# Kernel tuning notes

Measured on AMD Instinct MI355X. Metric: run time of the kernel, lower is better.

Reference implementation:

```python
import jax, jax.numpy as jnp
import numpy as np

N_NODES = 100000
N_EDGES = 1600000
N_FEAT = 128
HIDDEN = 128
N_CLASSES = 64


def setup_inputs() -> dict:
    key = jax.random.key(0)
    ks = jax.random.split(key, 6)
    x = jax.random.normal(ks[0], (N_NODES, N_FEAT), dtype=jnp.float32)
    edge_index = jax.random.randint(ks[1], (2, N_EDGES), 0, N_NODES, dtype=jnp.int64)
    # Glorot-ish scaled weights
    W1_l = jax.random.normal(ks[2], (N_FEAT, HIDDEN), dtype=jnp.float32) / np.sqrt(N_FEAT)
    W1_r = jax.random.normal(ks[3], (N_FEAT, HIDDEN), dtype=jnp.float32) / np.sqrt(N_FEAT)
    W2_l = jax.random.normal(ks[4], (HIDDEN, N_CLASSES), dtype=jnp.float32) / np.sqrt(HIDDEN)
    W2_r = jax.random.normal(ks[5], (HIDDEN, N_CLASSES), dtype=jnp.float32) / np.sqrt(HIDDEN)
    b1 = jnp.zeros((HIDDEN,), dtype=jnp.float32)
    b2 = jnp.zeros((N_CLASSES,), dtype=jnp.float32)
    return {"x": x, "edge_index": edge_index, "W1_l": W1_l, "b1": b1,
            "W1_r": W1_r, "W2_l": W2_l, "b2": b2, "W2_r": W2_r}


def _sage_conv(h, src, dst, n_nodes, inv_deg, W_l, W_r, b):
    # mean aggregation of source-node features into destination nodes
    agg = jax.ops.segment_sum(h[src], dst, num_segments=n_nodes)  # [N, d]
    agg = agg * inv_deg[:, None]
    return agg @ W_l + h @ W_r + b


def reference(x, edge_index, W1_l, b1, W1_r, W2_l, b2, W2_r):
    src, dst = edge_index[0], edge_index[1]
    n = x.shape[0]
    deg = jax.ops.segment_sum(jnp.ones_like(dst, dtype=x.dtype), dst, num_segments=n)
    inv_deg = 1.0 / jnp.maximum(deg, 1.0)
    h = jax.nn.relu(_sage_conv(x, src, dst, n, inv_deg, W1_l, W1_r, b1))
    # dropout is identity in eval mode
    out = _sage_conv(h, src, dst, n, inv_deg, W2_l, W2_r, b2)
    return out
```

## Files before the change

kernel.cpp:

```cpp
#include <hip/hip_runtime.h>

#define N_NODES   100000
#define N_EDGES   1600000
#define BSHIFT    9
#define NB        196

typedef __attribute__((ext_vector_type(8))) short short8;
typedef __attribute__((ext_vector_type(4))) float f32x4;
typedef __attribute__((ext_vector_type(2))) float f32x2;

__device__ __forceinline__ unsigned short f2bf(float f) {
    unsigned u = __float_as_uint(f);
    u += 0x7FFF + ((u >> 16) & 1);
    return (unsigned short)(u >> 16);
}

__device__ __forceinline__ int load_src(const int* e, int is64, int i) {
    return is64 ? e[2 * i] : e[i];
}
__device__ __forceinline__ int load_dst(const int* e, int is64, int i) {
    return is64 ? e[2 * (N_EDGES + i)] : e[N_EDGES + i];
}

__device__ __forceinline__ int block_detect_is64(const int* e, int* s_nz) {
    if (threadIdx.x == 0) *s_nz = 0;
    __syncthreads();
    int v = 0;
    for (int i = threadIdx.x; i < 1024; i += 256) v |= e[2 * i + 1];
    if (v) atomicOr(s_nz, 1);
    __syncthreads();
    return (*s_nz == 0) ? 1 : 0;
}

__global__ __launch_bounds__(256) void phaseA_kernel(
        const int* __restrict__ e, const float* __restrict__ x,
        const float* __restrict__ W1_l, const float* __restrict__ W1_r,
        const float* __restrict__ W2_l, const float* __restrict__ W2_r,
        int* __restrict__ bcnt, short* __restrict__ xb,
        unsigned int* __restrict__ xq,
        short* __restrict__ W1t, short* __restrict__ W2lt, short* __restrict__ W2rt) {
    const int blk = blockIdx.x;
    if (blk < 391) {
        __shared__ int s_nz;
        __shared__ int s_cnt[NB];
        for (int t = threadIdx.x; t < NB; t += 256) s_cnt[t] = 0;
        int is64 = block_detect_is64(e, &s_nz);
        __syncthreads();
        int i0 = blk * 4096;
        int n = min(4096, N_EDGES - i0);
        for (int t = 0; t < 16; t++) {
            int k = t * 256 + threadIdx.x;
            if (k < n) {
                int d = load_dst(e, is64, i0 + k);
                atomicAdd(&s_cnt[d >> BSHIFT], 1);
            }
        }
        __syncthreads();
        for (int t = threadIdx.x; t < NB; t += 256)
            if (s_cnt[t]) atomicAdd(&bcnt[t], s_cnt[t]);
    } else if (blk < 12891) {
        int t = (blk - 391) * 256 + threadIdx.x;
        int i = t * 4;
        float4 v = *(const float4*)&x[i];
        short4 o;
        o.x = (short)f2bf(v.x); o.y = (short)f2bf(v.y);
        o.z = (short)f2bf(v.z); o.w = (short)f2bf(v.w);
        *(short4*)&xb[i] = o;
        int w = __builtin_amdgcn_cvt_pk_fp8_f32(v.x, v.y, 0, false);
        w = __builtin_amdgcn_cvt_pk_fp8_f32(v.z, v.w, w, true);
        xq[t] = (unsigned int)w;
    } else {
        int i = (blk - 12891) * 256 + threadIdx.x;
        if (i < 32768) {
            int n = i >> 8, k = i & 255;
            float v = (k < 128) ? W1_l[k * 128 + n] : W1_r[(k - 128) * 128 + n];
            W1t[i] = (short)f2bf(v);
        } else if (i < 40960) {
            int j = i - 32768, n = j >> 7, k = j & 127;
            W2lt[j] = (short)f2bf(W2_l[k * 64 + n]);
        } else {
            int j = i - 40960, n = j >> 7, k = j & 127;
            W2rt[j] = (short)f2bf(W2_r[k * 64 + n]);
        }
    }
}

__global__ __launch_bounds__(256) void binscat_kernel(
        const int* __restrict__ e, const int* __restrict__ bcnt,
        int* __restrict__ boff, int* __restrict__ pairs) {
    __shared__ int2 s_pairs[4096];
    __shared__ int s_cnt[256], s_off[256], s_base[256], s_cur[256];
    __shared__ int s_nz;
    const int tid = threadIdx.x;
    s_cnt[tid] = 0;
    int is64 = block_detect_is64(e, &s_nz);
    __syncthreads();
    int i0 = blockIdx.x * 4096;
    int n = min(4096, N_EDGES - i0);
    int ls[16], ld[16];
    #pragma unroll
    for (int t = 0; t < 16; t++) {
        int k = t * 256 + tid;
        if (k < n) {
            ls[t] = load_src(e, is64, i0 + k);
            ld[t] = load_dst(e, is64, i0 + k);
            atomicAdd(&s_cnt[ld[t] >> BSHIFT], 1);
        }
    }
    __syncthreads();
    int lv = s_cnt[tid];
    s_off[tid] = lv;
    __syncthreads();
    for (int off = 1; off < 256; off <<= 1) {
        int t = (tid >= off) ? s_off[tid - off] : 0;
        __syncthreads();
        s_off[tid] += t;
        __syncthreads();
    }
    int excl = s_off[tid] - lv;
    int gv = (tid < NB) ? bcnt[tid] : 0;
    s_base[tid] = gv;
    __syncthreads();
    for (int off = 1; off < 256; off <<= 1) {
        int t = (tid >= off) ? s_base[tid - off] : 0;
        __syncthreads();
        s_base[tid] += t;
        __syncthreads();
    }
    int bst = s_base[tid] - gv;
    int gb = 0;
    if (tid < NB && lv > 0) gb = atomicAdd(&boff[tid], lv);
    s_off[tid] = excl;
    s_base[tid] = bst + gb;
    s_cur[tid] = excl;
    __syncthreads();
    #pragma unroll
    for (int t = 0; t < 16; t++) {
        int k = t * 256 + tid;
        if (k < n) {
            int pos = atomicAdd(&s_cur[ld[t] >> BSHIFT], 1);
            s_pairs[pos] = (int2){ls[t], ld[t]};
        }
    }
    __syncthreads();
    for (int j = tid; j < n; j += 256) {
        int2 pr = s_pairs[j];
        int b = pr.y >> BSHIFT;
        pairs[s_base[b] + (j - s_off[b])] = pr.x | ((pr.y & 511) << 17);
    }
}

__global__ __launch_bounds__(256) void fused_fill_kernel(
        const int* __restrict__ bcnt, const int* __restrict__ pairs,
        int* __restrict__ deg_i, int* __restrict__ cursor,
        float* __restrict__ inv_deg, int* __restrict__ col) {
    __shared__ int ldeg[512];
    __shared__ int ssum[256];
    __shared__ int sp0;
    const int tid = threadIdx.x;
    const int b = blockIdx.x;
    const int nbase = b << BSHIFT;
    int gv = (tid < NB) ? bcnt[tid] : 0;
    ssum[tid] = gv;
    __syncthreads();
    for (int off = 1; off < 256; off <<= 1) {
        int t = (tid >= off) ? ssum[tid - off] : 0;
        __syncthreads();
        ssum[tid] += t;
        __syncthreads();
    }
    if (tid == b) sp0 = ssum[tid] - gv;
    ldeg[tid] = 0; ldeg[tid + 256] = 0;
    __syncthreads();
    const int p0 = sp0, cnt = bcnt[b];
    for (int j = tid; j < cnt; j += 256)
        atomicAdd(&ldeg[pairs[p0 + j] >> 17], 1);
    __syncthreads();
    int d0 = ldeg[tid * 2], d1 = ldeg[tid * 2 + 1];
    int tsum = d0 + d1;
    ssum[tid] = tsum;
    __syncthreads();
    for (int off = 1; off < 256; off <<= 1) {
        int t = (tid >= off) ? ssum[tid - off] : 0;
        __syncthreads();
        ssum[tid] += t;
        __syncthreads();
    }
    int excl = ssum[tid] - tsum;
    int s0 = p0 + excl;
    int s1 = s0 + d0;
    ldeg[tid * 2] = s0;
    ldeg[tid * 2 + 1] = s1;
    int idx0 = nbase + tid * 2;
    if (idx0 < N_NODES) {
        deg_i[idx0] = d0;
        cursor[idx0] = s0;
        inv_deg[idx0] = 1.0f / fmaxf((float)d0, 1.0f);
    }
    if (idx0 + 1 < N_NODES) {
        deg_i[idx0 + 1] = d1;
        cursor[idx0 + 1] = s1;
        inv_deg[idx0 + 1] = 1.0f / fmaxf((float)d1, 1.0f);
    }
    __syncthreads();
    for (int j = tid; j < cnt; j += 256) {
        int pk = pairs[p0 + j];
        int pos = atomicAdd(&ldeg[pk >> 17], 1);
        col[pos] = pk & 0x1FFFF;
    }
}

__device__ __forceinline__ void acc_fp8x8(float* acc, uint2 w) {
    f32x2 f;
    f = __builtin_amdgcn_cvt_pk_f32_fp8((int)w.x, false); acc[0] += f[0]; acc[1] += f[1];
    f = __builtin_amdgcn_cvt_pk_f32_fp8((int)w.x, true);  acc[2] += f[0]; acc[3] += f[1];
    f = __builtin_amdgcn_cvt_pk_f32_fp8((int)w.y, false); acc[4] += f[0]; acc[5] += f[1];
    f = __builtin_amdgcn_cvt_pk_f32_fp8((int)w.y, true);  acc[6] += f[0]; acc[7] += f[1];
}

__global__ __launch_bounds__(256) void agg128_kernel(
        const int* __restrict__ cursor, const int* __restrict__ deg_i,
        const int* __restrict__ col, const unsigned int* __restrict__ xq,
        const float* __restrict__ inv_deg, short* __restrict__ agg) {
    int node = blockIdx.x * 16 + (threadIdx.x >> 4);
    int lane = threadIdx.x & 15;
    int cnt = deg_i[node];
    int start = cursor[node];
    float acc[8] = {0.f};
    int k = 0;
    for (; k + 4 <= cnt; k += 4) {
        int s0 = col[start + k + 0];
        int s1 = col[start + k + 1];
        int s2 = col[start + k + 2];
        int s3 = col[start + k + 3];
        uint2 w0 = *(const uint2*)(xq + (size_t)s0 * 32 + lane * 2);
        uint2 w1 = *(const uint2*)(xq + (size_t)s1 * 32 + lane * 2);
        uint2 w2 = *(const uint2*)(xq + (size_t)s2 * 32 + lane * 2);
        uint2 w3 = *(const uint2*)(xq + (size_t)s3 * 32 + lane * 2);
        acc_fp8x8(acc, w0); acc_fp8x8(acc, w1);
        acc_fp8x8(acc, w2); acc_fp8x8(acc, w3);
    }
    for (; k < cnt; k++) {
        int s0 = col[start + k];
        uint2 w = *(const uint2*)(xq + (size_t)s0 * 32 + lane * 2);
        acc_fp8x8(acc, w);
    }
    float sc = inv_deg[node];
    short8 o;
    #pragma unroll
    for (int j = 0; j < 8; j++) o[j] = (short)f2bf(acc[j] * sc);
    *(short8*)(agg + (size_t)node * 128 + lane * 8) = o;
}

__global__ __launch_bounds__(256) void agg64_kernel(
        const int* __restrict__ cursor, const int* __restrict__ deg_i,
        const int* __restrict__ col, const unsigned int* __restrict__ pq,
        const float* __restrict__ inv_deg, float* __restrict__ out) {
    int node = blockIdx.x * 32 + (threadIdx.x >> 3);
    int lane = threadIdx.x & 7;
    int cnt = deg_i[node];
    int start = cursor[node];
    float acc[8] = {0.f};
    int k = 0;
    for (; k + 4 <= cnt; k += 4) {
        int s0 = col[start + k + 0];
        int s1 = col[start + k + 1];
        int s2 = col[start + k + 2];
        int s3 = col[start + k + 3];
        uint2 w0 = *(const uint2*)(pq + (size_t)s0 * 16 + lane * 2);
        uint2 w1 = *(const uint2*)(pq + (size_t)s1 * 16 + lane * 2);
        uint2 w2 = *(const uint2*)(pq + (size_t)s2 * 16 + lane * 2);
        uint2 w3 = *(const uint2*)(pq + (size_t)s3 * 16 + lane * 2);
        acc_fp8x8(acc, w0); acc_fp8x8(acc, w1);
        acc_fp8x8(acc, w2); acc_fp8x8(acc, w3);
    }
    for (; k < cnt; k++) {
        int s0 = col[start + k];
        uint2 w = *(const uint2*)(pq + (size_t)s0 * 16 + lane * 2);
        acc_fp8x8(acc, w);
    }
    float sc = inv_deg[node];
    float* dst = out + (size_t)node * 64 + lane * 8;
    float4 o0 = *(float4*)dst;
    float4 o1 = *(float4*)(dst + 4);
    o0.x += acc[0] * sc; o0.y += acc[1] * sc; o0.z += acc[2] * sc; o0.w += acc[3] * sc;
    o1.x += acc[4] * sc; o1.y += acc[5] * sc; o1.z += acc[6] * sc; o1.w += acc[7] * sc;
    *(float4*)dst = o0;
    *(float4*)(dst + 4) = o1;
}

__global__ __launch_bounds__(256, 2) void gemm1_mfma(
        const short* __restrict__ agg1, const short* __restrict__ xb,
        const short* __restrict__ W1t, const float* __restrict__ b1,
        short* __restrict__ h) {
    const int wave = threadIdx.x >> 6, lane = threadIdx.x & 63;
    const int m = lane & 15, q = lane >> 4;
    const int wid = blockIdx.x * 4 + wave;
    const int half = wid & 1;
    short8 breg[4][8];
    #pragma unroll
    for (int t = 0; t < 4; t++)
        #pragma unroll
        for (int c = 0; c < 8; c++)
            breg[t][c] = *(const short8*)(W1t + (size_t)(half * 64 + t * 16 + m) * 256 + c * 32 + q * 8);
    float bias[4];
    #pragma unroll
    for (int t = 0; t < 4; t++) bias[t] = b1[half * 64 + t * 16 + m];

    for (int tile = wid >> 1; tile < 6250; tile += 1024) {
        const short* arow = agg1 + (size_t)(tile * 16 + m) * 128;
        const short* xrow = xb + (size_t)(tile * 16 + m) * 128;
        short8 a[8];
        #pragma unroll
        for (int c = 0; c < 4; c++) a[c] = *(const short8*)(arow + c * 32 + q * 8);
        #pragma unroll
        for (int c = 0; c < 4; c++) a[c + 4] = *(const short8*)(xrow + c * 32 + q * 8);
        f32x4 acc[4];
        #pragma unroll
        for (int t = 0; t < 4; t++) acc[t] = (f32x4){0.f, 0.f, 0.f, 0.f};
        #pragma unroll
        for (int c = 0; c < 8; c++)
            #pragma unroll
            for (int t = 0; t < 4; t++)
                acc[t] = __builtin_amdgcn_mfma_f32_16x16x32_bf16(a[c], breg[t][c], acc[t], 0, 0, 0);
        #pragma unroll
        for (int t = 0; t < 4; t++) {
            int colc = half * 64 + t * 16 + m;
            #pragma unroll
            for (int r = 0; r < 4; r++) {
                int rr = tile * 16 + q * 4 + r;
                h[(size_t)rr * 128 + colc] = (short)f2bf(fmaxf(acc[t][r] + bias[t], 0.f));
            }
        }
    }
}

__global__ __launch_bounds__(256, 2) void proj2_mfma(
        const short* __restrict__ h, const short* __restrict__ W2lt,
        const short* __restrict__ W2rt, const float* __restrict__ b2,
        unsigned char* __restrict__ p8, float* __restrict__ out) {
    const int wave = threadIdx.x >> 6, lane = threadIdx.x & 63;
    const int m = lane & 15, q = lane >> 4;
    const int wid = blockIdx.x * 4 + wave;
    short8 bl[4][4], br[4][4];
    #pragma unroll
    for (int t = 0; t < 4; t++)
        #pragma unroll
        for (int c = 0; c < 4; c++) {
            bl[t][c] = *(const short8*)(W2lt + (size_t)(t * 16 + m) * 128 + c * 32 + q * 8);
            br[t][c] = *(const short8*)(W2rt + (size_t)(t * 16 + m) * 128 + c * 32 + q * 8);
        }
    float bias[4];
    #pragma unroll
    for (int t = 0; t < 4; t++) bias[t] = b2[t * 16 + m];

    for (int tile = wid; tile < 6250; tile += 2048) {
        const short* hrow = h + (size_t)(tile * 16 + m) * 128;
        short8 a[4];
        #pragma unroll
        for (int c = 0; c < 4; c++) a[c] = *(const short8*)(hrow + c * 32 + q * 8);
        f32x4 accp[4], acco[4];
        #pragma unroll
        for (int t = 0; t < 4; t++) {
            accp[t] = (f32x4){0.f, 0.f, 0.f, 0.f};
            acco[t] = (f32x4){0.f, 0.f, 0.f, 0.f};
        }
        #pragma unroll
        for (int c = 0; c < 4; c++)
            #pragma unroll
            for (int t = 0; t < 4; t++) {
                accp[t] = __builtin_amdgcn_mfma_f32_16x16x32_bf16(a[c], bl[t][c], accp[t], 0, 0, 0);
                acco[t] = __builtin_amdgcn_mfma_f32_16x16x32_bf16(a[c], br[t][c], acco[t], 0, 0, 0);
            }
        #pragma unroll
        for (int t = 0; t < 4; t++) {
            int colc = t * 16 + m;
            #pragma unroll
            for (int r = 0; r < 4; r++) {
                int rr = tile * 16 + q * 4 + r;
                float pv = accp[t][r];
                int w = __builtin_amdgcn_cvt_pk_fp8_f32(pv, pv, 0, false);
                p8[(size_t)rr * 64 + colc] = (unsigned char)(w & 0xFF);
                out[(size_t)rr * 64 + colc] = acco[t][r] + bias[t];
            }
        }
    }
}

extern "C" void kernel_launch(void* const* d_in, const int* in_sizes, int n_in,
                              void* d_out, int out_size, void* d_ws, size_t ws_size,
                              hipStream_t stream) {
    const float* x    = (const float*)d_in[0];
    const int*   edge = (const int*)d_in[1];
    const float* W1_l = (const float*)d_in[2];
    const float* b1   = (const float*)d_in[3];
    const float* W1_r = (const float*)d_in[4];
    const float* W2_l = (const float*)d_in[5];
    const float* b2   = (const float*)d_in[6];
    const float* W2_r = (const float*)d_in[7];
    float* out = (float*)d_out;

    int* iw = (int*)d_ws;
    int* deg_i  = iw;
    int* cursor = iw + 100000;
    int* col    = iw + 200000;
    int* bcnt   = iw + 1800000;
    int* boff   = iw + 1800256;
    float* inv_deg = (float*)iw + 1800832;
    int*   pairs   = iw + 1900928;
    short* xb   = (short*)(iw + 3500928);
    short* hb   = xb + 12800000;
    short* ag1  = hb + 12800000;
    short* W1t  = ag1 + 12800000;
    short* W2lt = W1t + 32768;
    short* W2rt = W2lt + 8192;
    unsigned int* xq = (unsigned int*)hb;
    unsigned char* p8 = (unsigned char*)ag1;
    unsigned int*  pq = (unsigned int*)ag1;

    hipMemsetAsync(bcnt, 0, 512 * sizeof(int), stream);

    phaseA_kernel<<<13083, 256, 0, stream>>>(edge, x, W1_l, W1_r, W2_l, W2_r,
                                             bcnt, xb, xq, W1t, W2lt, W2rt);
    binscat_kernel<<<391, 256, 0, stream>>>(edge, bcnt, boff, pairs);
    fused_fill_kernel<<<NB, 256, 0, stream>>>(bcnt, pairs, deg_i, cursor, inv_deg, col);

    agg128_kernel<<<6250, 256, 0, stream>>>(cursor, deg_i, col, xq, inv_deg, ag1);
    gemm1_mfma<<<512, 256, 0, stream>>>(ag1, xb, W1t, b1, hb);

    proj2_mfma<<<512, 256, 0, stream>>>(hb, W2lt, W2rt, b2, p8, out);
    agg64_kernel<<<3125, 256, 0, stream>>>(cursor, deg_i, col, pq, inv_deg, out);
}
```

Measured before the change: 267.5 us.

## Fold edge bucketing into phaseA with fixed-stride bucket slots, prefetch GEMM tiles

The separate count pass and the binscat kernel are merged: phaseA blocks now bin edges directly into fixed-capacity bucket regions (BSTRIDE per bucket), each claimed through an atomic cursor. This drops one kernel launch and a second full read of the edge list. The fill kernel moves to 512 threads, one node per thread, and the col array uses the padded bucket layout. gemm1 and proj2 also software-prefetch the next tile's A operands. The risk is that a bucket with more edges than its fixed capacity would overflow, and phaseA's larger static shared memory may lower occupancy for the conversion blocks.

```diff
diff --git a/kernel.cpp b/kernel.cpp
--- a/kernel.cpp
+++ b/kernel.cpp
@@ -4,6 +4,7 @@
 #define N_EDGES   1600000
 #define BSHIFT    9
 #define NB        196
+#define BSTRIDE   9216
 
 typedef __attribute__((ext_vector_type(8))) short short8;
 typedef __attribute__((ext_vector_type(4))) float f32x4;
@@ -36,28 +37,61 @@
         const int* __restrict__ e, const float* __restrict__ x,
         const float* __restrict__ W1_l, const float* __restrict__ W1_r,
         const float* __restrict__ W2_l, const float* __restrict__ W2_r,
-        int* __restrict__ bcnt, short* __restrict__ xb,
-        unsigned int* __restrict__ xq,
+        int* __restrict__ bktcur, int* __restrict__ pairs,
+        short* __restrict__ xb, unsigned int* __restrict__ xq,
         short* __restrict__ W1t, short* __restrict__ W2lt, short* __restrict__ W2rt) {
+    __shared__ int2 s_pairs[4096];
+    __shared__ int s_cnt[256], s_off[256], s_base[256], s_cur[256];
+    __shared__ int s_nz;
     const int blk = blockIdx.x;
     if (blk < 391) {
-        __shared__ int s_nz;
-        __shared__ int s_cnt[NB];
-        for (int t = threadIdx.x; t < NB; t += 256) s_cnt[t] = 0;
+        const int tid = threadIdx.x;
+        s_cnt[tid] = 0;
         int is64 = block_detect_is64(e, &s_nz);
         __syncthreads();
         int i0 = blk * 4096;
         int n = min(4096, N_EDGES - i0);
+        int ls[16], ld[16];
+        #pragma unroll
         for (int t = 0; t < 16; t++) {
-            int k = t * 256 + threadIdx.x;
+            int k = t * 256 + tid;
             if (k < n) {
-                int d = load_dst(e, is64, i0 + k);
-                atomicAdd(&s_cnt[d >> BSHIFT], 1);
-            }
-        }
-        __syncthreads();
-        for (int t = threadIdx.x; t < NB; t += 256)
-            if (s_cnt[t]) atomicAdd(&bcnt[t], s_cnt[t]);
+                ls[t] = load_src(e, is64, i0 + k);
+                ld[t] = load_dst(e, is64, i0 + k);
+                atomicAdd(&s_cnt[ld[t] >> BSHIFT], 1);
+            }
+        }
+        __syncthreads();
+        int lv = s_cnt[tid];
+        s_off[tid] = lv;
+        __syncthreads();
+        for (int off = 1; off < 256; off <<= 1) {
+            int t = (tid >= off) ? s_off[tid - off] : 0;
+            __syncthreads();
+            s_off[tid] += t;
+            __syncthreads();
+        }
+        int excl = s_off[tid] - lv;
+        int gb = 0;
+        if (tid < NB && lv > 0) gb = atomicAdd(&bktcur[tid], lv);
+        s_off[tid] = excl;
+        s_base[tid] = tid * BSTRIDE + gb;
+        s_cur[tid] = excl;
+        __syncthreads();
+        #pragma unroll
+        for (int t = 0; t < 16; t++) {
+            int k = t * 256 + tid;
+            if (k < n) {
+                int pos = atomicAdd(&s_cur[ld[t] >> BSHIFT], 1);
+                s_pairs[pos] = (int2){ls[t], ld[t]};
+            }
+        }
+        __syncthreads();
+        for (int j = tid; j < n; j += 256) {
+            int2 pr = s_pairs[j];
+            int b = pr.y >> BSHIFT;
+            pairs[s_base[b] + (j - s_off[b])] = pr.x | ((pr.y & 511) << 17);
+        }
     } else if (blk < 12891) {
         int t = (blk - 391) * 256 + threadIdx.x;
         int i = t * 4;
@@ -85,125 +119,41 @@
     }
 }
 
-__global__ __launch_bounds__(256) void binscat_kernel(
-        const int* __restrict__ e, const int* __restrict__ bcnt,
-        int* __restrict__ boff, int* __restrict__ pairs) {
-    __shared__ int2 s_pairs[4096];
-    __shared__ int s_cnt[256], s_off[256], s_base[256], s_cur[256];
-    __shared__ int s_nz;
-    const int tid = threadIdx.x;
-    s_cnt[tid] = 0;
-    int is64 = block_detect_is64(e, &s_nz);
-    __syncthreads();
-    int i0 = blockIdx.x * 4096;
-    int n = min(4096, N_EDGES - i0);
-    int ls[16], ld[16];
-    #pragma unroll
-    for (int t = 0; t < 16; t++) {
-        int k = t * 256 + tid;
-        if (k < n) {
-            ls[t] = load_src(e, is64, i0 + k);
-            ld[t] = load_dst(e, is64, i0 + k);
-            atomicAdd(&s_cnt[ld[t] >> BSHIFT], 1);
-        }
-    }
-    __syncthreads();
-    int lv = s_cnt[tid];
-    s_off[tid] = lv;
-    __syncthreads();
-    for (int off = 1; off < 256; off <<= 1) {
-        int t = (tid >= off) ? s_off[tid - off] : 0;
-        __syncthreads();
-        s_off[tid] += t;
-        __syncthreads();
-    }
-    int excl = s_off[tid] - lv;
-    int gv = (tid < NB) ? bcnt[tid] : 0;
-    s_base[tid] = gv;
-    __syncthreads();
-    for (int off = 1; off < 256; off <<= 1) {
-        int t = (tid >= off) ? s_base[tid - off] : 0;
-        __syncthreads();
-        s_base[tid] += t;
-        __syncthreads();
-    }
-    int bst = s_base[tid] - gv;
-    int gb = 0;
-    if (tid < NB && lv > 0) gb = atomicAdd(&boff[tid], lv);
-    s_off[tid] = excl;
-    s_base[tid] = bst + gb;
-    s_cur[tid] = excl;
-    __syncthreads();
-    #pragma unroll
-    for (int t = 0; t < 16; t++) {
-        int k = t * 256 + tid;
-        if (k < n) {
-            int pos = atomicAdd(&s_cur[ld[t] >> BSHIFT], 1);
-            s_pairs[pos] = (int2){ls[t], ld[t]};
-        }
-    }
-    __syncthreads();
-    for (int j = tid; j < n; j += 256) {
-        int2 pr = s_pairs[j];
-        int b = pr.y >> BSHIFT;
-        pairs[s_base[b] + (j - s_off[b])] = pr.x | ((pr.y & 511) << 17);
-    }
-}
-
-__global__ __launch_bounds__(256) void fused_fill_kernel(
-        const int* __restrict__ bcnt, const int* __restrict__ pairs,
+__global__ __launch_bounds__(512) void fused_fill_kernel(
+        const int* __restrict__ bktcur, const int* __restrict__ pairs,
         int* __restrict__ deg_i, int* __restrict__ cursor,
         float* __restrict__ inv_deg, int* __restrict__ col) {
     __shared__ int ldeg[512];
-    __shared__ int ssum[256];
-    __shared__ int sp0;
+    __shared__ int ssum[512];
     const int tid = threadIdx.x;
     const int b = blockIdx.x;
     const int nbase = b << BSHIFT;
-    int gv = (tid < NB) ? bcnt[tid] : 0;
-    ssum[tid] = gv;
-    __syncthreads();
-    for (int off = 1; off < 256; off <<= 1) {
+    ldeg[tid] = 0;
+    __syncthreads();
+    const int cnt = bktcur[b];
+    const int p0 = b * BSTRIDE;
+    for (int j = tid; j < cnt; j += 512)
+        atomicAdd(&ldeg[pairs[p0 + j] >> 17], 1);
+    __syncthreads();
+    int d = ldeg[tid];
+    ssum[tid] = d;
+    __syncthreads();
+    for (int off = 1; off < 512; off <<= 1) {
         int t = (tid >= off) ? ssum[tid - off] : 0;
         __syncthreads();
         ssum[tid] += t;
         __syncthreads();
     }
-    if (tid == b) sp0 = ssum[tid] - gv;
-    ldeg[tid] = 0; ldeg[tid + 256] = 0;
-    __syncthreads();
-    const int p0 = sp0, cnt = bcnt[b];
-    for (int j = tid; j < cnt; j += 256)
-        atomicAdd(&ldeg[pairs[p0 + j] >> 17], 1);
-    __syncthreads();
-    int d0 = ldeg[tid * 2], d1 = ldeg[tid * 2 + 1];
-    int tsum = d0 + d1;
-    ssum[tid] = tsum;
-    __syncthreads();
-    for (int off = 1; off < 256; off <<= 1) {
-        int t = (tid >= off) ? ssum[tid - off] : 0;
-        __syncthreads();
-        ssum[tid] += t;
-        __syncthreads();
-    }
-    int excl = ssum[tid] - tsum;
-    int s0 = p0 + excl;
-    int s1 = s0 + d0;
-    ldeg[tid * 2] = s0;
-    ldeg[tid * 2 + 1] = s1;
-    int idx0 = nbase + tid * 2;
-    if (idx0 < N_NODES) {
-        deg_i[idx0] = d0;
-        cursor[idx0] = s0;
-        inv_deg[idx0] = 1.0f / fmaxf((float)d0, 1.0f);
-    }
-    if (idx0 + 1 < N_NODES) {
-        deg_i[idx0 + 1] = d1;
-        cursor[idx0 + 1] = s1;
-        inv_deg[idx0 + 1] = 1.0f / fmaxf((float)d1, 1.0f);
-    }
-    __syncthreads();
-    for (int j = tid; j < cnt; j += 256) {
+    int s = p0 + ssum[tid] - d;
+    int node = nbase + tid;
+    if (node < N_NODES) {
+        deg_i[node] = d;
+        cursor[node] = s;
+        inv_deg[node] = 1.0f / fmaxf((float)d, 1.0f);
+    }
+    ldeg[tid] = s;
+    __syncthreads();
+    for (int j = tid; j < cnt; j += 512) {
         int pk = pairs[p0 + j];
         int pos = atomicAdd(&ldeg[pk >> 17], 1);
         col[pos] = pk & 0x1FFFF;
@@ -307,14 +257,30 @@
     #pragma unroll
     for (int t = 0; t < 4; t++) bias[t] = b1[half * 64 + t * 16 + m];
 
-    for (int tile = wid >> 1; tile < 6250; tile += 1024) {
+    int tile = wid >> 1;
+    if (tile >= 6250) return;
+    short8 a[8];
+    {
         const short* arow = agg1 + (size_t)(tile * 16 + m) * 128;
         const short* xrow = xb + (size_t)(tile * 16 + m) * 128;
-        short8 a[8];
-        #pragma unroll
-        for (int c = 0; c < 4; c++) a[c] = *(const short8*)(arow + c * 32 + q * 8);
-        #pragma unroll
-        for (int c = 0; c < 4; c++) a[c + 4] = *(const short8*)(xrow + c * 32 + q * 8);
+        #pragma unroll
+        for (int c = 0; c < 4; c++) {
+            a[c]     = *(const short8*)(arow + c * 32 + q * 8);
+            a[c + 4] = *(const short8*)(xrow + c * 32 + q * 8);
+        }
+    }
+    while (true) {
+        int nt = tile + 1024;
+        short8 an[8];
+        if (nt < 6250) {
+            const short* arow = agg1 + (size_t)(nt * 16 + m) * 128;
+            const short* xrow = xb + (size_t)(nt * 16 + m) * 128;
+            #pragma unroll
+            for (int c = 0; c < 4; c++) {
+                an[c]     = *(const short8*)(arow + c * 32 + q * 8);
+                an[c + 4] = *(const short8*)(xrow + c * 32 + q * 8);
+            }
+        }
         f32x4 acc[4];
         #pragma unroll
         for (int t = 0; t < 4; t++) acc[t] = (f32x4){0.f, 0.f, 0.f, 0.f};
@@ -332,6 +298,10 @@
                 h[(size_t)rr * 128 + colc] = (short)f2bf(fmaxf(acc[t][r] + bias[t], 0.f));
             }
         }
+        if (nt >= 6250) break;
+        #pragma unroll
+        for (int c = 0; c < 8; c++) a[c] = an[c];
+        tile = nt;
     }
 }
 
@@ -354,11 +324,22 @@
     #pragma unroll
     for (int t = 0; t < 4; t++) bias[t] = b2[t * 16 + m];
 
-    for (int tile = wid; tile < 6250; tile += 2048) {
+    int tile = wid;
+    if (tile >= 6250) return;
+    short8 a[4];
+    {
         const short* hrow = h + (size_t)(tile * 16 + m) * 128;
-        short8 a[4];
         #pragma unroll
         for (int c = 0; c < 4; c++) a[c] = *(const short8*)(hrow + c * 32 + q * 8);
+    }
+    while (true) {
+        int nt = tile + 2048;
+        short8 an[4];
+        if (nt < 6250) {
+            const short* hrow = h + (size_t)(nt * 16 + m) * 128;
+            #pragma unroll
+            for (int c = 0; c < 4; c++) an[c] = *(const short8*)(hrow + c * 32 + q * 8);
+        }
         f32x4 accp[4], acco[4];
         #pragma unroll
         for (int t = 0; t < 4; t++) {
@@ -384,6 +365,10 @@
                 out[(size_t)rr * 64 + colc] = acco[t][r] + bias[t];
             }
         }
+        if (nt >= 6250) break;
+        #pragma unroll
+        for (int c = 0; c < 4; c++) a[c] = an[c];
+        tile = nt;
     }
 }
 
@@ -403,27 +388,25 @@
     int* iw = (int*)d_ws;
     int* deg_i  = iw;
     int* cursor = iw + 100000;
-    int* col    = iw + 200000;
-    int* bcnt   = iw + 1800000;
-    int* boff   = iw + 1800256;
-    float* inv_deg = (float*)iw + 1800832;
-    int*   pairs   = iw + 1900928;
-    short* xb   = (short*)(iw + 3500928);
+    int* bktcur = iw + 200000;
+    float* inv_deg = (float*)(iw + 200256);
+    int* col    = iw + 300352;
+    short* xb   = (short*)(iw + 2106688);
     short* hb   = xb + 12800000;
     short* ag1  = hb + 12800000;
     short* W1t  = ag1 + 12800000;
     short* W2lt = W1t + 32768;
     short* W2rt = W2lt + 8192;
     unsigned int* xq = (unsigned int*)hb;
+    int* pairs = (int*)ag1;
     unsigned char* p8 = (unsigned char*)ag1;
     unsigned int*  pq = (unsigned int*)ag1;
 
-    hipMemsetAsync(bcnt, 0, 512 * sizeof(int), stream);
+    hipMemsetAsync(bktcur, 0, 256 * sizeof(int), stream);
 
     phaseA_kernel<<<13083, 256, 0, stream>>>(edge, x, W1_l, W1_r, W2_l, W2_r,
-                                             bcnt, xb, xq, W1t, W2lt, W2rt);
-    binscat_kernel<<<391, 256, 0, stream>>>(edge, bcnt, boff, pairs);
-    fused_fill_kernel<<<NB, 256, 0, stream>>>(bcnt, pairs, deg_i, cursor, inv_deg, col);
+                                             bktcur, pairs, xb, xq, W1t, W2lt, W2rt);
+    fused_fill_kernel<<<NB, 512, 0, stream>>>(bktcur, pairs, deg_i, cursor, inv_deg, col);
 
     agg128_kernel<<<6250, 256, 0, stream>>>(cursor, deg_i, col, xq, inv_deg, ag1);
     gemm1_mfma<<<512, 256, 0, stream>>>(ag1, xb, W1t, b1, hb);
```

Result: faster. 246.3 us (-7.9%).
